# Kernel optimization log

Hardware: AMD Instinct MI355X
Metric: run time of the kernel (lower is better)

The kernel has to match this reference:

```python
import jax, jax.numpy as jnp
import numpy as np

Nc, Ns, Nt, d_h, BS = 64, 64, 64, 128, 16


def setup_inputs() -> dict:
    key = jax.random.key(0)
    k1, k2, k3, k4, k5 = jax.random.split(key, 5)
    Ac = (jax.random.uniform(k1, (Ns, Nc)) < 0.05).astype(jnp.float32)
    As = (jax.random.uniform(k2, (Ns, Ns)) < 0.05).astype(jnp.float32)
    # AA = As@As@Ac + As@Ac + Ac, then binarize (masked_fill(AA != 0, 1))
    AA = As @ As @ Ac + As @ Ac + Ac
    AA = (AA != 0).astype(jnp.float32)                 # [Ns, Nc]
    AA_mask = jnp.tile(AA, (Nt, Nt))                   # [Ns*Nt, Nc*Nt], == AA.repeat(Nt,Nt) in torch
    GCW = jax.random.normal(k3, (Ns * Nt, Nc * Nt), dtype=jnp.float32)
    GCB = jax.random.normal(k4, (Ns * Nt, d_h), dtype=jnp.float32)
    h = jax.random.normal(k5, (BS, Nc, Nt, d_h), dtype=jnp.float32)
    e = jnp.zeros((1,), jnp.float32)                   # unused in forward (kept for signature parity)
    return {"h": h, "e": e, "AA_mask": AA_mask, "GCW": GCW, "GCB": GCB}


def reference(h, e, AA_mask, GCW, GCB):
    bs = h.shape[0]
    # A = relu(AA.repeat(Nt,Nt) * GCW)  -- structured masked weight [Ns*Nt, Nc*Nt]
    A = jax.nn.relu(AA_mask * GCW)
    # h: [bs, Nc, Nt, d_h] -> [bs, Nt, Nc, d_h] -> [bs, Nt*Nc, d_h]
    x = jnp.transpose(h, (0, 2, 1, 3)).reshape(bs, Nt * Nc, d_h)
    # relu(A @ x + GCB): [bs, Ns*Nt, d_h]
    x = jax.nn.relu(jnp.einsum('ij,bjd->bid', A, x) + GCB)
    # [bs, Nt, Ns, d_h] -> [bs, Ns, Nt, d_h] (final torch reshape is a no-op)
    x = x.reshape(bs, Nt, Ns, d_h)
    x = jnp.transpose(x, (0, 2, 1, 3))
    return x
```

## Files before the change

kernel.cpp:

```cpp
#include <hip/hip_runtime.h>


#define NC 64
#define NS 64
#define NT 64
#define DH 128
#define BATCH 16
#define MDIM 4096
#define KDIM 4096
#define TM 128
#define TK 64
#define BM 128
#define BN 256
#define BK 64
#define NTILES (KDIM / BK)

typedef __attribute__((ext_vector_type(8))) short short8;
typedef __attribute__((ext_vector_type(4))) float floatx4;

__device__ __forceinline__ unsigned short f2bf(float f) {
    union { float f; unsigned int i; } v; v.f = f;
    return (unsigned short)((v.i + 0x7fffu + ((v.i >> 16) & 1u)) >> 16);
}
__device__ __forceinline__ void async16(const void* g, void* l) {
    __builtin_amdgcn_global_load_lds(
        (const __attribute__((address_space(1))) void*)g,
        (__attribute__((address_space(3))) void*)l, 16, 0, 0);
}

__global__ __launch_bounds__(256)
void prep(const float* __restrict__ aam, const float* __restrict__ gcw,
          const float* __restrict__ hmat,
          unsigned short* __restrict__ Abf, unsigned short* __restrict__ XT)
{
    const int tid = threadIdx.x;
    if ((int)blockIdx.x < MDIM) {
        const int i = blockIdx.x;
        __shared__ float sm[64];
        if (tid < 64) sm[tid] = aam[(size_t)(i & 63) * KDIM + tid];
        __syncthreads();
        const size_t base = (size_t)i * KDIM + tid * 16;
        floatx4 w0 = *(const floatx4*)(gcw + base);
        floatx4 w1 = *(const floatx4*)(gcw + base + 4);
        floatx4 w2 = *(const floatx4*)(gcw + base + 8);
        floatx4 w3 = *(const floatx4*)(gcw + base + 12);
        const float* m = &sm[(tid & 3) * 16];
        short8 p0, p1;
#pragma unroll
        for (int e = 0; e < 4; ++e) {
            float v0 = m[e]      * w0[e]; v0 = v0 > 0.f ? v0 : 0.f;
            float v1 = m[e + 4]  * w1[e]; v1 = v1 > 0.f ? v1 : 0.f;
            float v2 = m[e + 8]  * w2[e]; v2 = v2 > 0.f ? v2 : 0.f;
            float v3 = m[e + 12] * w3[e]; v3 = v3 > 0.f ? v3 : 0.f;
            p0[e]     = (short)f2bf(v0);
            p0[e + 4] = (short)f2bf(v1);
            p1[e]     = (short)f2bf(v2);
            p1[e + 4] = (short)f2bf(v3);
        }
        *(short8*)(Abf + base)     = p0;
        *(short8*)(Abf + base + 8) = p1;
    } else {
        const int blk = blockIdx.x - MDIM;
        const int b = blk >> 6;
        const int t = blk & 63;
        const int c0 = (tid & 7) * 8;
        const int d0 = tid >> 3;
#pragma unroll
        for (int it = 0; it < 4; ++it) {
            const int d = d0 + it * 32;
            short8 p;
#pragma unroll
            for (int e = 0; e < 8; ++e) {
                float v = hmat[(((size_t)b * NC + (c0 + e)) * NT + t) * DH + d];
                p[e] = (short)f2bf(v);
            }
            *(short8*)(XT + ((size_t)(b * DH + d)) * KDIM + t * 64 + c0) = p;
        }
    }
}

__global__ __launch_bounds__(512, 2)
void gemm(const unsigned short* __restrict__ Abf,
          const unsigned short* __restrict__ XT,
          const float* __restrict__ gcb,
          float* __restrict__ out)
{
    __shared__ short lds[3][(BM + BN) * BK];

    const int tid = threadIdx.x;
    const int bid = blockIdx.x;
    const int np  = bid & 7;
    const int mp  = bid >> 3;
    const int i0  = mp * BM;
    const int n0  = np * BN;

    const int lane = tid & 63;
    const int w    = tid >> 6;
    const int wm   = (w >> 2) * 64;
    const int wn   = (w & 3) * 64;
    const int l15  = lane & 15;
    const int q    = lane >> 4;

    const int srow = lane >> 3;
    const int swz  = ((lane & 7) ^ srow) << 3;

    const unsigned short* Ab = Abf + (size_t)i0 * KDIM + swz;
    const unsigned short* Xb = XT  + (size_t)n0 * KDIM + swz;

    floatx4 acc[4][4];
#pragma unroll
    for (int mi = 0; mi < 4; ++mi)
#pragma unroll
        for (int ni = 0; ni < 4; ++ni)
            acc[mi][ni] = (floatx4){0.f, 0.f, 0.f, 0.f};

    auto stage = [&](int t, int b) {
        const int k0 = t * BK;
        short* dst = lds[b];
#pragma unroll
        for (int ii = 0; ii < 2; ++ii) {
            const int r = ii * 64 + w * 8 + srow;
            async16(Ab + (size_t)r * KDIM + k0, dst + (ii * 64 + w * 8) * BK);
        }
#pragma unroll
        for (int ii = 0; ii < 4; ++ii) {
            const int r = ii * 64 + w * 8 + srow;
            async16(Xb + (size_t)r * KDIM + k0, dst + (BM + ii * 64 + w * 8) * BK);
        }
    };

    auto compute = [&](int b) {
        const short* sA = lds[b];
        const short* sX = lds[b] + BM * BK;
#pragma unroll
        for (int h = 0; h < 2; ++h) {
            const int co = ((h * 4 + q) ^ (l15 & 7)) << 3;
            short8 af[4], xf[4];
#pragma unroll
            for (int mi = 0; mi < 4; ++mi)
                af[mi] = *(const short8*)&sA[(wm + mi * 16 + l15) * BK + co];
#pragma unroll
            for (int ni = 0; ni < 4; ++ni)
                xf[ni] = *(const short8*)&sX[(wn + ni * 16 + l15) * BK + co];
            __builtin_amdgcn_s_setprio(1);
#pragma unroll
            for (int mi = 0; mi < 4; ++mi)
#pragma unroll
                for (int ni = 0; ni < 4; ++ni)
                    acc[mi][ni] = __builtin_amdgcn_mfma_f32_16x16x32_bf16(
                        af[mi], xf[ni], acc[mi][ni], 0, 0, 0);
            __builtin_amdgcn_s_setprio(0);
        }
    };

    stage(0, 0);
    stage(1, 1);

    int bc = 0;
    for (int t = 0; t < NTILES - 1; ++t) {
        asm volatile("s_waitcnt vmcnt(6)" ::: "memory");
        __builtin_amdgcn_s_barrier();
        asm volatile("" ::: "memory");
        int bs = bc + 2; if (bs >= 3) bs -= 3;
        if (t + 2 < NTILES) stage(t + 2, bs);
        compute(bc);
        if (++bc == 3) bc = 0;
    }
    asm volatile("s_waitcnt vmcnt(0)" ::: "memory");
    __builtin_amdgcn_s_barrier();
    asm volatile("" ::: "memory");
    compute(bc);

#pragma unroll
    for (int mi = 0; mi < 4; ++mi) {
        const int ibase = i0 + wm + mi * 16 + q * 4;
#pragma unroll
        for (int ni = 0; ni < 4; ++ni) {
            const int n  = n0 + wn + ni * 16 + l15;
            const int bb = n >> 7;
            const int d  = n & 127;
#pragma unroll
            for (int r = 0; r < 4; ++r) {
                const int i = ibase + r;
                float v = acc[mi][ni][r] + gcb[(size_t)i * DH + d];
                v = v > 0.f ? v : 0.f;
                out[(((size_t)bb * NS + (i & 63)) * NT + (i >> 6)) * DH + d] = v;
            }
        }
    }
}

#define APAD 40
#define XPAD 20
__global__ __launch_bounds__(256, 2)
void gcn_fused(const float* __restrict__ hmat, const float* __restrict__ aam,
               const float* __restrict__ gcw, const float* __restrict__ gcb,
               float* __restrict__ out)
{
    __shared__ short sA[TM * APAD];
    __shared__ unsigned int sX[DH * XPAD];
    const int tid = threadIdx.x;
    const int bid = blockIdx.x;
    const int mp  = (bid & 7) * 4 + (bid >> 7);
    const int b   = (bid >> 3) & 15;
    const int i0  = mp * TM;
    const int lane = tid & 63;
    const int wm = ((tid >> 6) >> 1) * 64;
    const int wn = ((tid >> 6) & 1) * 64;
    const int l15 = lane & 15;
    const int q   = lane >> 4;
    floatx4 acc[4][4];
#pragma unroll
    for (int mi = 0; mi < 4; ++mi)
#pragma unroll
        for (int ni = 0; ni < 4; ++ni) acc[mi][ni] = (floatx4){0.f,0.f,0.f,0.f};
    const int ar = tid >> 2, ac = (tid & 3) << 3;
    const int kp = tid >> 4, dg = (tid & 15) << 3;
    const int wkey = (tid & 3) << 2;
    for (int k0 = 0; k0 < KDIM; k0 += 32) {
        const size_t ga0 = (size_t)(i0 + ar) * KDIM + (k0 + ac);
        const size_t ga1 = ga0 + (size_t)64 * KDIM;
        floatx4 aa0a = *(const floatx4*)(aam + ga0), aa0b = *(const floatx4*)(aam + ga0 + 4);
        floatx4 ww0a = *(const floatx4*)(gcw + ga0), ww0b = *(const floatx4*)(gcw + ga0 + 4);
        floatx4 aa1a = *(const floatx4*)(aam + ga1), aa1b = *(const floatx4*)(aam + ga1 + 4);
        floatx4 ww1a = *(const floatx4*)(gcw + ga1), ww1b = *(const floatx4*)(gcw + ga1 + 4);
        const int jj = k0 + 2 * kp, tt = jj >> 6, cc = jj & 63;
        const size_t gx0 = ((size_t)(b * NC + cc) * NT + tt) * DH + dg;
        const size_t gx1 = gx0 + (size_t)NT * DH;
        floatx4 x0a = *(const floatx4*)(hmat + gx0), x0b = *(const floatx4*)(hmat + gx0 + 4);
        floatx4 x1a = *(const floatx4*)(hmat + gx1), x1b = *(const floatx4*)(hmat + gx1 + 4);
        __syncthreads();
        short8 p0, p1;
#pragma unroll
        for (int e = 0; e < 4; ++e) {
            float v0 = aa0a[e]*ww0a[e]; v0 = v0>0.f?v0:0.f;
            float v1 = aa0b[e]*ww0b[e]; v1 = v1>0.f?v1:0.f;
            float v2 = aa1a[e]*ww1a[e]; v2 = v2>0.f?v2:0.f;
            float v3 = aa1b[e]*ww1b[e]; v3 = v3>0.f?v3:0.f;
            p0[e] = (short)f2bf(v0); p0[e+4] = (short)f2bf(v1);
            p1[e] = (short)f2bf(v2); p1[e+4] = (short)f2bf(v3);
        }
        *(short8*)&sA[ar * APAD + ac] = p0;
        *(short8*)&sA[(ar + 64) * APAD + ac] = p1;
#pragma unroll
        for (int e = 0; e < 4; ++e) {
            unsigned int pka = (unsigned int)f2bf(x0a[e]) | ((unsigned int)f2bf(x1a[e]) << 16);
            unsigned int pkb = (unsigned int)f2bf(x0b[e]) | ((unsigned int)f2bf(x1b[e]) << 16);
            sX[(dg + e) * XPAD + (kp ^ wkey)] = pka;
            sX[(dg + e + 4) * XPAD + (kp ^ wkey)] = pkb;
        }
        __syncthreads();
        short8 afrag[4], bfrag[4];
#pragma unroll
        for (int mi = 0; mi < 4; ++mi)
            afrag[mi] = *(const short8*)&sA[(wm + mi * 16 + l15) * APAD + q * 8];
#pragma unroll
        for (int ni = 0; ni < 4; ++ni) {
            const int row = wn + ni * 16 + l15;
            const int col = (q * 4) ^ (((row >> 3) & 3) << 2);
            bfrag[ni] = *(const short8*)(sX + row * XPAD + col);
        }
#pragma unroll
        for (int mi = 0; mi < 4; ++mi)
#pragma unroll
            for (int ni = 0; ni < 4; ++ni)
                acc[mi][ni] = __builtin_amdgcn_mfma_f32_16x16x32_bf16(
                    afrag[mi], bfrag[ni], acc[mi][ni], 0, 0, 0);
    }
#pragma unroll
    for (int mi = 0; mi < 4; ++mi) {
        const int ibase = i0 + wm + mi * 16 + q * 4;
#pragma unroll
        for (int ni = 0; ni < 4; ++ni) {
            const int d = wn + ni * 16 + l15;
#pragma unroll
            for (int r = 0; r < 4; ++r) {
                const int i = ibase + r;
                float v = acc[mi][ni][r] + gcb[(size_t)i * DH + d];
                v = v > 0.f ? v : 0.f;
                out[(((size_t)b * NS + (i & 63)) * NT + (i >> 6)) * DH + d] = v;
            }
        }
    }
}

extern "C" void kernel_launch(void* const* d_in, const int* in_sizes, int n_in,
                              void* d_out, int out_size, void* d_ws, size_t ws_size,
                              hipStream_t stream) {
    const float* h   = (const float*)d_in[0];
    const float* aam = (const float*)d_in[2];
    const float* gcw = (const float*)d_in[3];
    const float* gcb = (const float*)d_in[4];
    float* out = (float*)d_out;

    const size_t A_BYTES  = (size_t)MDIM * KDIM * 2;
    const size_t XT_BYTES = (size_t)BATCH * DH * KDIM * 2;

    if (ws_size >= A_BYTES + XT_BYTES) {
        unsigned short* Abf = (unsigned short*)d_ws;
        unsigned short* XT  = (unsigned short*)((char*)d_ws + A_BYTES);
        prep<<<dim3(MDIM + BATCH * NT), 256, 0, stream>>>(aam, gcw, h, Abf, XT);
        gemm<<<dim3((MDIM / BM) * (BATCH * DH / BN)), 512, 0, stream>>>(Abf, XT, gcb, out);
    } else {
        gcn_fused<<<dim3((MDIM / TM) * BATCH), 256, 0, stream>>>(h, aam, gcw, gcb, out);
    }
}
```

Before: 237.0 us.

## Interleave async global loads with MFMA sub-steps in main K loop

Replaces the stage-then-compute sequence in the main loop with a hand-scheduled two-phase body. Each phase loads LDS fragments for half of the K tile, issues half of the async global-to-LDS copies for the tile two steps ahead, then runs MFMAs between extra barriers. The aim is to spread global load issue across the compute so memory and matrix work overlap better. The extra workgroup barriers per iteration add synchronisation cost.

Measured after the change: 238.7 us. About the same (+0.7%).

```diff
diff --git a/kernel.cpp b/kernel.cpp
--- a/kernel.cpp
+++ b/kernel.cpp
@@ -158,12 +158,66 @@
 
     int bc = 0;
     for (int t = 0; t < NTILES - 1; ++t) {
+        const short* sA = lds[bc];
+        const short* sX = sA + BM * BK;
+        int bs = bc + 2; if (bs >= 3) bs -= 3;
+        short* dst = lds[bs];
+        const int k2 = (t + 2) * BK;
+        const bool st = (t + 2 < NTILES);
+
         asm volatile("s_waitcnt vmcnt(6)" ::: "memory");
         __builtin_amdgcn_s_barrier();
-        asm volatile("" ::: "memory");
-        int bs = bc + 2; if (bs >= 3) bs -= 3;
-        if (t + 2 < NTILES) stage(t + 2, bs);
-        compute(bc);
+
+        short8 af[4], xf[4];
+        {
+            const int co = (q ^ (l15 & 7)) << 3;
+#pragma unroll
+            for (int mi = 0; mi < 4; ++mi)
+                af[mi] = *(const short8*)&sA[(wm + mi * 16 + l15) * BK + co];
+#pragma unroll
+            for (int ni = 0; ni < 4; ++ni)
+                xf[ni] = *(const short8*)&sX[(wn + ni * 16 + l15) * BK + co];
+        }
+        if (st) {
+            async16(Ab + (size_t)(w * 8 + srow) * KDIM + k2,        dst + (w * 8) * BK);
+            async16(Ab + (size_t)(64 + w * 8 + srow) * KDIM + k2,   dst + (64 + w * 8) * BK);
+            async16(Xb + (size_t)(w * 8 + srow) * KDIM + k2,        dst + (BM + w * 8) * BK);
+        }
+        __builtin_amdgcn_s_barrier();
+        __builtin_amdgcn_s_setprio(1);
+#pragma unroll
+        for (int mi = 0; mi < 4; ++mi)
+#pragma unroll
+            for (int ni = 0; ni < 4; ++ni)
+                acc[mi][ni] = __builtin_amdgcn_mfma_f32_16x16x32_bf16(
+                    af[mi], xf[ni], acc[mi][ni], 0, 0, 0);
+        __builtin_amdgcn_s_setprio(0);
+        __builtin_amdgcn_s_barrier();
+
+        {
+            const int co = ((4 + q) ^ (l15 & 7)) << 3;
+#pragma unroll
+            for (int mi = 0; mi < 4; ++mi)
+                af[mi] = *(const short8*)&sA[(wm + mi * 16 + l15) * BK + co];
+#pragma unroll
+            for (int ni = 0; ni < 4; ++ni)
+                xf[ni] = *(const short8*)&sX[(wn + ni * 16 + l15) * BK + co];
+        }
+        if (st) {
+            async16(Xb + (size_t)(64 + w * 8 + srow) * KDIM + k2,   dst + (BM + 64 + w * 8) * BK);
+            async16(Xb + (size_t)(128 + w * 8 + srow) * KDIM + k2,  dst + (BM + 128 + w * 8) * BK);
+            async16(Xb + (size_t)(192 + w * 8 + srow) * KDIM + k2,  dst + (BM + 192 + w * 8) * BK);
+        }
+        __builtin_amdgcn_s_barrier();
+        __builtin_amdgcn_s_setprio(1);
+#pragma unroll
+        for (int mi = 0; mi < 4; ++mi)
+#pragma unroll
+            for (int ni = 0; ni < 4; ++ni)
+                acc[mi][ni] = __builtin_amdgcn_mfma_f32_16x16x32_bf16(
+                    af[mi], xf[ni], acc[mi][ni], 0, 0, 0);
+        __builtin_amdgcn_s_setprio(0);
+
         if (++bc == 3) bc = 0;
     }
     asm volatile("s_waitcnt vmcnt(0)" ::: "memory");
```

## Exploit block-sparse mask structure to skip zero K tiles in GEMM

Applied to the files above, without the earlier changes.

The mask is AA tiled, so row s of the output depends only on the nonzero columns c of AA[s]. The prep kernel now compacts each mask row's nonzero column indices, permutes A rows by (s, t) and packs only the active K-blocks. The GEMM then iterates only over the active blocks of each s, using a smaller 64-row tile with double buffering, and gathers X tiles by column index. The X transpose also goes through LDS for coalesced access. This cuts GEMM work in proportion to mask density, at the cost of an uneven per-block loop count and a reduced pipeline depth.

After: 229.3 us. -3.2%, faster.

```diff
diff --git a/kernel.cpp b/kernel.cpp
--- a/kernel.cpp
+++ b/kernel.cpp
@@ -8,14 +8,15 @@
 #define BATCH 16
 #define MDIM 4096
 #define KDIM 4096
+#define KPAD 4096
 #define TM 128
 #define TK 64
-#define BM 128
-#define BN 256
-#define BK 64
-#define NTILES (KDIM / BK)
+#define GBM 64
+#define GBN 256
+#define GBK 64
 
 typedef __attribute__((ext_vector_type(8))) short short8;
+typedef __attribute__((ext_vector_type(4))) short short4v;
 typedef __attribute__((ext_vector_type(4))) float floatx4;
 
 __device__ __forceinline__ unsigned short f2bf(float f) {
@@ -31,81 +32,114 @@
 __global__ __launch_bounds__(256)
 void prep(const float* __restrict__ aam, const float* __restrict__ gcw,
           const float* __restrict__ hmat,
-          unsigned short* __restrict__ Abf, unsigned short* __restrict__ XT)
+          unsigned short* __restrict__ Abf, unsigned short* __restrict__ XT,
+          unsigned short* __restrict__ cidx, int* __restrict__ nsb)
 {
     const int tid = threadIdx.x;
     if ((int)blockIdx.x < MDIM) {
-        const int i = blockIdx.x;
-        __shared__ float sm[64];
-        if (tid < 64) sm[tid] = aam[(size_t)(i & 63) * KDIM + tid];
+        const int r  = blockIdx.x;
+        const int s  = r >> 6;
+        const int tt = r & 63;
+        const int i  = tt * 64 + s;
+        __shared__ unsigned short scidx[64];
+        __shared__ int sns;
+        __shared__ unsigned short srow[4096];
+        if (tid < 64) {
+            float v = aam[(size_t)s * KDIM + tid];
+            unsigned long long m = __ballot(v != 0.f);
+            int rank = __popcll(m & ((1ull << tid) - 1ull));
+            if (v != 0.f) scidx[rank] = (unsigned short)tid;
+            if (tid == 0) sns = (int)__popcll(m);
+            if (tt == 0) {
+                if (v != 0.f) cidx[s * 64 + rank] = (unsigned short)tid;
+                if (tid == 0) nsb[s] = (int)__popcll(m);
+            }
+        }
+        const float* gr = gcw + (size_t)i * KDIM;
+#pragma unroll
+        for (int u = 0; u < 4; ++u) {
+            const int idx = u * 1024 + tid * 4;
+            floatx4 wv = *(const floatx4*)(gr + idx);
+            short4v p;
+#pragma unroll
+            for (int e = 0; e < 4; ++e) {
+                float v = wv[e] > 0.f ? wv[e] : 0.f;
+                p[e] = (short)f2bf(v);
+            }
+            *(short4v*)&srow[idx] = p;
+        }
         __syncthreads();
-        const size_t base = (size_t)i * KDIM + tid * 16;
-        floatx4 w0 = *(const floatx4*)(gcw + base);
-        floatx4 w1 = *(const floatx4*)(gcw + base + 4);
-        floatx4 w2 = *(const floatx4*)(gcw + base + 8);
-        floatx4 w3 = *(const floatx4*)(gcw + base + 12);
-        const float* m = &sm[(tid & 3) * 16];
-        short8 p0, p1;
-#pragma unroll
-        for (int e = 0; e < 4; ++e) {
-            float v0 = m[e]      * w0[e]; v0 = v0 > 0.f ? v0 : 0.f;
-            float v1 = m[e + 4]  * w1[e]; v1 = v1 > 0.f ? v1 : 0.f;
-            float v2 = m[e + 8]  * w2[e]; v2 = v2 > 0.f ? v2 : 0.f;
-            float v3 = m[e + 12] * w3[e]; v3 = v3 > 0.f ? v3 : 0.f;
-            p0[e]     = (short)f2bf(v0);
-            p0[e + 4] = (short)f2bf(v1);
-            p1[e]     = (short)f2bf(v2);
-            p1[e + 4] = (short)f2bf(v3);
-        }
-        *(short8*)(Abf + base)     = p0;
-        *(short8*)(Abf + base + 8) = p1;
+        const int ke = sns * 64;
+        for (int kk0 = tid * 8; kk0 < ke; kk0 += 2048) {
+            const int c  = (int)scidx[kk0 >> 6];
+            const int t0 = kk0 & 63;
+            short8 p;
+#pragma unroll
+            for (int e = 0; e < 8; ++e)
+                p[e] = (short)srow[(t0 + e) * 64 + c];
+            *(short8*)(Abf + (size_t)r * KPAD + kk0) = p;
+        }
     } else {
         const int blk = blockIdx.x - MDIM;
         const int b = blk >> 6;
-        const int t = blk & 63;
-        const int c0 = (tid & 7) * 8;
-        const int d0 = tid >> 3;
-#pragma unroll
-        for (int it = 0; it < 4; ++it) {
-            const int d = d0 + it * 32;
+        const int c = blk & 63;
+        __shared__ unsigned short sx[64][136];
+        const float* hp = hmat + (((size_t)b * NC + c) * NT) * DH;
+#pragma unroll
+        for (int u = 0; u < 8; ++u) {
+            const int idx = u * 1024 + tid * 4;
+            const int t = idx >> 7;
+            const int d = idx & 127;
+            floatx4 v = *(const floatx4*)(hp + idx);
+            short4v p;
+#pragma unroll
+            for (int e = 0; e < 4; ++e) p[e] = (short)f2bf(v[e]);
+            *(short4v*)&sx[t][d] = p;
+        }
+        __syncthreads();
+        const int d  = tid >> 1;
+        const int th = (tid & 1) * 32;
+        unsigned short* dst = XT + ((size_t)(b * DH + d)) * KPAD + c * 64 + th;
+#pragma unroll
+        for (int u2 = 0; u2 < 4; ++u2) {
             short8 p;
 #pragma unroll
-            for (int e = 0; e < 8; ++e) {
-                float v = hmat[(((size_t)b * NC + (c0 + e)) * NT + t) * DH + d];
-                p[e] = (short)f2bf(v);
-            }
-            *(short8*)(XT + ((size_t)(b * DH + d)) * KDIM + t * 64 + c0) = p;
-        }
-    }
-}
-
-__global__ __launch_bounds__(512, 2)
+            for (int e = 0; e < 8; ++e)
+                p[e] = (short)sx[th + u2 * 8 + e][d];
+            *(short8*)(dst + u2 * 8) = p;
+        }
+    }
+}
+
+__global__ __launch_bounds__(256, 2)
 void gemm(const unsigned short* __restrict__ Abf,
           const unsigned short* __restrict__ XT,
+          const unsigned short* __restrict__ cidx,
+          const int* __restrict__ nsb,
           const float* __restrict__ gcb,
           float* __restrict__ out)
 {
-    __shared__ short lds[3][(BM + BN) * BK];
+    __shared__ short lds[2][(GBM + GBN) * GBK];
 
     const int tid = threadIdx.x;
     const int bid = blockIdx.x;
-    const int np  = bid & 7;
-    const int mp  = bid >> 3;
-    const int i0  = mp * BM;
-    const int n0  = np * BN;
+    const int np = bid & 7;
+    const int s  = bid >> 3;
+    const int n0 = np * GBN;
 
     const int lane = tid & 63;
     const int w    = tid >> 6;
-    const int wm   = (w >> 2) * 64;
-    const int wn   = (w & 3) * 64;
+    const int wn   = w * 64;
     const int l15  = lane & 15;
     const int q    = lane >> 4;
-
     const int srow = lane >> 3;
     const int swz  = ((lane & 7) ^ srow) << 3;
 
-    const unsigned short* Ab = Abf + (size_t)i0 * KDIM + swz;
-    const unsigned short* Xb = XT  + (size_t)n0 * KDIM + swz;
+    const int nt = nsb[s];
+    const int cl = (int)cidx[s * 64 + lane];
+
+    const unsigned short* Ab = Abf + (size_t)(s * 64) * KPAD + swz;
+    const unsigned short* Xb = XT  + (size_t)n0 * KPAD + swz;
 
     floatx4 acc[4][4];
 #pragma unroll
@@ -115,33 +149,32 @@
             acc[mi][ni] = (floatx4){0.f, 0.f, 0.f, 0.f};
 
     auto stage = [&](int t, int b) {
-        const int k0 = t * BK;
         short* dst = lds[b];
-#pragma unroll
-        for (int ii = 0; ii < 2; ++ii) {
-            const int r = ii * 64 + w * 8 + srow;
-            async16(Ab + (size_t)r * KDIM + k0, dst + (ii * 64 + w * 8) * BK);
-        }
-#pragma unroll
-        for (int ii = 0; ii < 4; ++ii) {
-            const int r = ii * 64 + w * 8 + srow;
-            async16(Xb + (size_t)r * KDIM + k0, dst + (BM + ii * 64 + w * 8) * BK);
+        const int c = __shfl(cl, t);
+        const size_t ka = (size_t)t * GBK;
+        const size_t kx = (size_t)c * GBK;
+        async16(Ab + (size_t)(w * 8 + srow) * KPAD + ka,       dst + (w * 8) * GBK);
+        async16(Ab + (size_t)((w + 4) * 8 + srow) * KPAD + ka, dst + ((w + 4) * 8) * GBK);
+#pragma unroll
+        for (int g = 0; g < 8; ++g) {
+            const int rr = w * 64 + g * 8;
+            async16(Xb + (size_t)(rr + srow) * KPAD + kx, dst + (GBM + rr) * GBK);
         }
     };
 
     auto compute = [&](int b) {
         const short* sA = lds[b];
-        const short* sX = lds[b] + BM * BK;
-#pragma unroll
-        for (int h = 0; h < 2; ++h) {
-            const int co = ((h * 4 + q) ^ (l15 & 7)) << 3;
+        const short* sX = lds[b] + GBM * GBK;
+#pragma unroll
+        for (int h2 = 0; h2 < 2; ++h2) {
+            const int co = ((h2 * 4 + q) ^ (l15 & 7)) << 3;
             short8 af[4], xf[4];
 #pragma unroll
             for (int mi = 0; mi < 4; ++mi)
-                af[mi] = *(const short8*)&sA[(wm + mi * 16 + l15) * BK + co];
+                af[mi] = *(const short8*)&sA[(mi * 16 + l15) * GBK + co];
 #pragma unroll
             for (int ni = 0; ni < 4; ++ni)
-                xf[ni] = *(const short8*)&sX[(wn + ni * 16 + l15) * BK + co];
+                xf[ni] = *(const short8*)&sX[(wn + ni * 16 + l15) * GBK + co];
             __builtin_amdgcn_s_setprio(1);
 #pragma unroll
             for (int mi = 0; mi < 4; ++mi)
@@ -153,27 +186,24 @@
         }
     };
 
-    stage(0, 0);
-    stage(1, 1);
-
-    int bc = 0;
-    for (int t = 0; t < NTILES - 1; ++t) {
-        asm volatile("s_waitcnt vmcnt(6)" ::: "memory");
+    if (nt > 0) stage(0, 0);
+    if (nt > 1) stage(1, 1);
+    for (int t = 0; t < nt - 1; ++t) {
+        asm volatile("s_waitcnt vmcnt(10)" ::: "memory");
         __builtin_amdgcn_s_barrier();
-        asm volatile("" ::: "memory");
-        int bs = bc + 2; if (bs >= 3) bs -= 3;
-        if (t + 2 < NTILES) stage(t + 2, bs);
-        compute(bc);
-        if (++bc == 3) bc = 0;
-    }
-    asm volatile("s_waitcnt vmcnt(0)" ::: "memory");
-    __builtin_amdgcn_s_barrier();
-    asm volatile("" ::: "memory");
-    compute(bc);
+        compute(t & 1);
+        __builtin_amdgcn_s_barrier();
+        if (t + 2 < nt) stage(t + 2, t & 1);
+    }
+    if (nt > 0) {
+        asm volatile("s_waitcnt vmcnt(0)" ::: "memory");
+        __builtin_amdgcn_s_barrier();
+        compute((nt - 1) & 1);
+    }
 
 #pragma unroll
     for (int mi = 0; mi < 4; ++mi) {
-        const int ibase = i0 + wm + mi * 16 + q * 4;
+        const int tt0 = mi * 16 + q * 4;
 #pragma unroll
         for (int ni = 0; ni < 4; ++ni) {
             const int n  = n0 + wn + ni * 16 + l15;
@@ -181,10 +211,11 @@
             const int d  = n & 127;
 #pragma unroll
             for (int r = 0; r < 4; ++r) {
-                const int i = ibase + r;
+                const int tt = tt0 + r;
+                const int i  = tt * 64 + s;
                 float v = acc[mi][ni][r] + gcb[(size_t)i * DH + d];
                 v = v > 0.f ? v : 0.f;
-                out[(((size_t)bb * NS + (i & 63)) * NT + (i >> 6)) * DH + d] = v;
+                out[(((size_t)bb * NS + s) * NT + tt) * DH + d] = v;
             }
         }
     }
@@ -293,14 +324,18 @@
     const float* gcb = (const float*)d_in[4];
     float* out = (float*)d_out;
 
-    const size_t A_BYTES  = (size_t)MDIM * KDIM * 2;
-    const size_t XT_BYTES = (size_t)BATCH * DH * KDIM * 2;
-
-    if (ws_size >= A_BYTES + XT_BYTES) {
+    const size_t A_BYTES   = (size_t)MDIM * KPAD * 2;
+    const size_t XT_BYTES  = (size_t)BATCH * DH * KPAD * 2;
+    const size_t IDX_BYTES = 64 * 64 * 2;
+    const size_t NS_BYTES  = 64 * 4;
+
+    if (ws_size >= A_BYTES + XT_BYTES + IDX_BYTES + NS_BYTES) {
         unsigned short* Abf = (unsigned short*)d_ws;
-        unsigned short* XT  = (unsigned short*)((char*)d_ws + A_BYTES);
-        prep<<<dim3(MDIM + BATCH * NT), 256, 0, stream>>>(aam, gcw, h, Abf, XT);
-        gemm<<<dim3((MDIM / BM) * (BATCH * DH / BN)), 512, 0, stream>>>(Abf, XT, gcb, out);
+        unsigned short* XTp = (unsigned short*)((char*)d_ws + A_BYTES);
+        unsigned short* cid = (unsigned short*)((char*)d_ws + A_BYTES + XT_BYTES);
+        int* nsb            = (int*)((char*)d_ws + A_BYTES + XT_BYTES + IDX_BYTES);
+        prep<<<dim3(MDIM + BATCH * NT), 256, 0, stream>>>(aam, gcw, h, Abf, XTp, cid, nsb);
+        gemm<<<dim3(64 * 8), 256, 0, stream>>>(Abf, XTp, cid, nsb, gcb, out);
     } else {
         gcn_fused<<<dim3((MDIM / TM) * BATCH), 256, 0, stream>>>(h, aam, gcw, gcb, out);
     }
```
